# Optimization experiments

Hardware: AMD Instinct MI355X
Metric: run time of the kernel (lower is better)

## Reference

```python
import jax, jax.numpy as jnp
import numpy as np

GROUPSIZE = 128
IN_F, OUT_F = 4096, 11008
TOKENS = 512


def setup_inputs() -> dict:
    key = jax.random.key(0)
    k1, k2, k3, k4, k5 = jax.random.split(key, 5)
    x = jax.random.normal(k1, (TOKENS, IN_F), dtype=jnp.float32)
    # packed 4-bit codes: two nibbles per byte, stored as int32 in [0, 256)
    qweight = jax.random.randint(k2, (OUT_F * IN_F // 2,), 0, 256, dtype=jnp.int32)
    n_groups = OUT_F * IN_F // GROUPSIZE
    scales = jax.random.uniform(k3, (n_groups, 1), dtype=jnp.float32) * 0.02 + 1e-3
    zeros = jax.random.uniform(k4, (n_groups, 1), dtype=jnp.float32) * 15.0
    bias = jax.random.normal(k5, (OUT_F,), dtype=jnp.float32)
    return {"x": x, "qweight": qweight, "scales": scales, "zeros": zeros, "bias": bias}


def _dequant_w4(qweight, scales, zeros, dtype):
    # python_decompress: high nibble then low nibble, each in [0,16)
    hi = (qweight >> 4) % 16
    lo = qweight % 16
    codes = jnp.stack([hi, lo], axis=-1).reshape(-1, GROUPSIZE).astype(dtype)
    # group-wise dequant: (code - zero) * scale, zeros/scales are (n_groups, 1)
    w = (codes - zeros.astype(dtype)) * scales.astype(dtype)
    return w.reshape(OUT_F, IN_F)


def reference(x, qweight, scales, zeros, bias):
    w = _dequant_w4(qweight, scales, zeros, x.dtype)  # [out, in]
    return x @ w.T + bias
```

## Files before the change

kernel.cpp:

```cpp
#include <hip/hip_runtime.h>

#define GROUPSIZE 128
#define IN_F 4096
#define OUT_F 11008
#define TOKENS 512
#define N_GROUPS (OUT_F * IN_F / GROUPSIZE)

#define BM 64
#define BN 128
#define BK 64
#define NTHREADS 256
#define NT (IN_F / BK)

typedef _Float16 half8  __attribute__((ext_vector_type(8)));
typedef _Float16 half2v __attribute__((ext_vector_type(2)));
typedef float    f32x4  __attribute__((ext_vector_type(4)));
typedef int      ivec4  __attribute__((ext_vector_type(4)));

__device__ __forceinline__ int swz(int r, int k) {
    return ((r << 6) + k) ^ ((r & 7) << 3);
}

__device__ __forceinline__ void glds16(const _Float16* g, _Float16* l) {
    __builtin_amdgcn_global_load_lds(
        (const __attribute__((address_space(1))) void*)g,
        (__attribute__((address_space(3))) void*)l, 16, 0, 0);
}

__global__ __launch_bounds__(256)
void cvt_x_kernel(const float* __restrict__ x, _Float16* __restrict__ x16) {
    size_t i = ((size_t)blockIdx.x * 256 + threadIdx.x) * 8;
    f32x4 a = *(const f32x4*)(x + i);
    f32x4 b = *(const f32x4*)(x + i + 4);
    half8 h;
    h[0]=(_Float16)a[0]; h[1]=(_Float16)a[1]; h[2]=(_Float16)a[2]; h[3]=(_Float16)a[3];
    h[4]=(_Float16)b[0]; h[5]=(_Float16)b[1]; h[6]=(_Float16)b[2]; h[7]=(_Float16)b[3];
    *(half8*)(x16 + i) = h;
}

__global__ __launch_bounds__(256)
void szpack_kernel(const float* __restrict__ s, const float* __restrict__ z,
                   uint2* __restrict__ szp) {
    int g = blockIdx.x * 256 + threadIdx.x;
    if (g >= N_GROUPS) return;
    _Float16 S = (_Float16)s[g];
    _Float16 B = (_Float16)(-(64.0f + z[g]) * (float)S);
    unsigned short su = __builtin_bit_cast(unsigned short, S);
    unsigned short bu = __builtin_bit_cast(unsigned short, B);
    uint2 r;
    r.x = ((unsigned)su << 16) | su;
    r.y = ((unsigned)bu << 16) | bu;
    szp[g] = r;
}

__device__ __forceinline__ half8 dq8(ivec4 q, uint2 sz) {
    half2v S  = __builtin_bit_cast(half2v, sz.x);
    half2v Bv = __builtin_bit_cast(half2v, sz.y);
    half8 r;
#pragma unroll
    for (int e = 0; e < 4; ++e) {
        unsigned qq = (unsigned)q[e];
        unsigned u = ((qq & 0xF0u) | ((qq << 20) & 0x00F00000u)) | 0x54005400u;
        half2v h = __builtin_bit_cast(half2v, u);
        half2v w = h * S + Bv;
        r[2*e]   = w[0];
        r[2*e+1] = w[1];
    }
    return r;
}

__global__ __launch_bounds__(NTHREADS, 3)
void qlinear_main(const _Float16* __restrict__ x16,
                  const int*   __restrict__ qw,
                  const uint2* __restrict__ szp,
                  const float* __restrict__ bias,
                  float*       __restrict__ out)
{
    __shared__ __align__(16) _Float16 As[2][BM * BK];
    __shared__ __align__(16) _Float16 Bs[2][BN * BK];

    const int tid = threadIdx.x;
    const int n0 = blockIdx.x * BN;
    const int m0 = blockIdx.y * BM;
    const int wv = tid >> 6, ln = tid & 63;

    const int brow = tid & 127;
    const int bh   = tid >> 7;
    const int* qg = qw + (size_t)(n0 + brow) * (IN_F / 2) + bh * 16;
    const int szbase = (n0 + brow) * (IN_F / GROUPSIZE);

    const int ar  = wv * 16 + (ln >> 3);
    const int gsw = (ln & 7) ^ ((ln >> 3) & 7);
    const _Float16* ag = x16 + (size_t)(m0 + ar) * IN_F + gsw * 8;

    const int wr = (wv >> 1) * 32, wc = (wv & 1) * 64;
    const int lr = ln & 15, lk8 = (ln >> 4) * 8, lk4 = (ln >> 4) * 4;

    f32x4 acc[2][4];
#pragma unroll
    for (int i = 0; i < 2; ++i)
#pragma unroll
        for (int j = 0; j < 4; ++j)
            acc[i][j] = (f32x4){0.f, 0.f, 0.f, 0.f};

#define LOAD_Q(qs, szs, tt) do {                                   \
        const ivec4* qp = (const ivec4*)(qg + (tt) * 32);          \
        qs[0] = qp[0]; qs[1] = qp[1]; qs[2] = qp[2]; qs[3] = qp[3];\
        szs = szp[szbase + ((tt) >> 1)];                           \
    } while (0)

#define STAGE_A(tt, buf) do {                                      \
        const _Float16* gp = ag + (size_t)(tt) * 64;               \
        glds16(gp,             &As[buf][wv * 1024]);               \
        glds16(gp + 8 * IN_F,  &As[buf][wv * 1024 + 512]);         \
    } while (0)

#define DQ_STORE(qs, szs, buf) do {                                        \
        *(half8*)&Bs[buf][swz(brow, bh * 32 + 0)]  = dq8(qs[0], szs);      \
        *(half8*)&Bs[buf][swz(brow, bh * 32 + 8)]  = dq8(qs[1], szs);      \
        *(half8*)&Bs[buf][swz(brow, bh * 32 + 16)] = dq8(qs[2], szs);      \
        *(half8*)&Bs[buf][swz(brow, bh * 32 + 24)] = dq8(qs[3], szs);      \
    } while (0)

    auto mfma_phase = [&](int buf) {
#pragma unroll
        for (int kk = 0; kk < 2; ++kk) {
            half8 af[2], bf[4];
#pragma unroll
            for (int i = 0; i < 2; ++i)
                af[i] = *(const half8*)&As[buf][swz(wr + i * 16 + lr, kk * 32 + lk8)];
#pragma unroll
            for (int j = 0; j < 4; ++j)
                bf[j] = *(const half8*)&Bs[buf][swz(wc + j * 16 + lr, kk * 32 + lk8)];
#pragma unroll
            for (int i = 0; i < 2; ++i)
#pragma unroll
                for (int j = 0; j < 4; ++j)
                    acc[i][j] = __builtin_amdgcn_mfma_f32_16x16x32_f16(
                        af[i], bf[j], acc[i][j], 0, 0, 0);
        }
    };

    ivec4 qA[4], qB[4];
    uint2 szA, szB;
    LOAD_Q(qA, szA, 0);
    LOAD_Q(qB, szB, 1);
    STAGE_A(0, 0);
    DQ_STORE(qA, szA, 0);
    __syncthreads();

    for (int t = 0; t < NT; t += 2) {
        {
            const int tl = (t + 2 < NT) ? t + 2 : NT - 1;
            LOAD_Q(qA, szA, tl);
            STAGE_A((t + 1 < NT) ? t + 1 : NT - 1, 1);
            DQ_STORE(qB, szB, 1);
            mfma_phase(0);
            __syncthreads();
        }
        {
            const int tl = (t + 3 < NT) ? t + 3 : NT - 1;
            LOAD_Q(qB, szB, tl);
            STAGE_A((t + 2 < NT) ? t + 2 : NT - 1, 0);
            DQ_STORE(qA, szA, 0);
            mfma_phase(1);
            __syncthreads();
        }
    }

#pragma unroll
    for (int j = 0; j < 4; ++j) {
        const int col = n0 + wc + j * 16 + lr;
        const float bv = bias[col];
#pragma unroll
        for (int i = 0; i < 2; ++i) {
            const int rb = m0 + wr + i * 16 + lk4;
#pragma unroll
            for (int r = 0; r < 4; ++r)
                out[(size_t)(rb + r) * OUT_F + col] = acc[i][j][r] + bv;
        }
    }
#undef LOAD_Q
#undef STAGE_A
#undef DQ_STORE
}

extern "C" void kernel_launch(void* const* d_in, const int* in_sizes, int n_in,
                              void* d_out, int out_size, void* d_ws, size_t ws_size,
                              hipStream_t stream) {
    const float* x      = (const float*)d_in[0];
    const int*   qw     = (const int*)d_in[1];
    const float* scales = (const float*)d_in[2];
    const float* zeros  = (const float*)d_in[3];
    const float* bias   = (const float*)d_in[4];
    float*       out    = (float*)d_out;

    _Float16* x16 = (_Float16*)d_ws;
    uint2*    szp = (uint2*)((char*)d_ws + (size_t)TOKENS * IN_F * 2);

    cvt_x_kernel<<<TOKENS * IN_F / (256 * 8), 256, 0, stream>>>(x, x16);
    szpack_kernel<<<(N_GROUPS + 255) / 256, 256, 0, stream>>>(scales, zeros, szp);

    dim3 grid(OUT_F / BN, TOKENS / BM);
    qlinear_main<<<grid, NTHREADS, 0, stream>>>(x16, qw, szp, bias, out);
}
```

Baseline: 312.1 us.

## Coalesce packed weight loads and swap grid order for weight reuse

Weight loading is remapped so that 8 consecutive threads read contiguous 16-byte chunks of one row, covering 32 rows per pass with four passes, instead of each thread reading 64 contiguous bytes of its own row. Each thread now keeps four scale/zero pairs, one per row. The grid is also transposed so that the M-blocks sharing one N-tile are launched next to each other, which should improve L2 reuse of the quantized weights across token blocks. Register use goes up slightly because of the per-row scale/zero values.

Result: faster. 255.0 us (-18.3%).

```diff
diff --git a/kernel.cpp b/kernel.cpp
--- a/kernel.cpp
+++ b/kernel.cpp
@@ -80,14 +80,14 @@
     __shared__ __align__(16) _Float16 Bs[2][BN * BK];
 
     const int tid = threadIdx.x;
-    const int n0 = blockIdx.x * BN;
-    const int m0 = blockIdx.y * BM;
+    const int m0 = blockIdx.x * BM;
+    const int n0 = blockIdx.y * BN;
     const int wv = tid >> 6, ln = tid & 63;
 
-    const int brow = tid & 127;
-    const int bh   = tid >> 7;
-    const int* qg = qw + (size_t)(n0 + brow) * (IN_F / 2) + bh * 16;
-    const int szbase = (n0 + brow) * (IN_F / GROUPSIZE);
+    const int s8 = tid & 7;
+    const int r0 = tid >> 3;
+    const int* qg = qw + (size_t)(n0 + r0) * (IN_F / 2) + s8 * 4;
+    const int szb = (n0 + r0) * (IN_F / GROUPSIZE);
 
     const int ar  = wv * 16 + (ln >> 3);
     const int gsw = (ln & 7) ^ ((ln >> 3) & 7);
@@ -103,10 +103,12 @@
         for (int j = 0; j < 4; ++j)
             acc[i][j] = (f32x4){0.f, 0.f, 0.f, 0.f};
 
-#define LOAD_Q(qs, szs, tt) do {                                   \
-        const ivec4* qp = (const ivec4*)(qg + (tt) * 32);          \
-        qs[0] = qp[0]; qs[1] = qp[1]; qs[2] = qp[2]; qs[3] = qp[3];\
-        szs = szp[szbase + ((tt) >> 1)];                           \
+#define LOAD_Q(qs, szs, tt) do {                                            \
+        _Pragma("unroll")                                                   \
+        for (int j = 0; j < 4; ++j) {                                       \
+            qs[j]  = *(const ivec4*)(qg + (size_t)j * 32 * (IN_F/2) + (tt) * 32); \
+            szs[j] = szp[szb + j * 32 * (IN_F/GROUPSIZE) + ((tt) >> 1)];    \
+        }                                                                   \
     } while (0)
 
 #define STAGE_A(tt, buf) do {                                      \
@@ -116,10 +118,9 @@
     } while (0)
 
 #define DQ_STORE(qs, szs, buf) do {                                        \
-        *(half8*)&Bs[buf][swz(brow, bh * 32 + 0)]  = dq8(qs[0], szs);      \
-        *(half8*)&Bs[buf][swz(brow, bh * 32 + 8)]  = dq8(qs[1], szs);      \
-        *(half8*)&Bs[buf][swz(brow, bh * 32 + 16)] = dq8(qs[2], szs);      \
-        *(half8*)&Bs[buf][swz(brow, bh * 32 + 24)] = dq8(qs[3], szs);      \
+        _Pragma("unroll")                                                  \
+        for (int j = 0; j < 4; ++j)                                        \
+            *(half8*)&Bs[buf][swz(r0 + 32 * j, s8 * 8)] = dq8(qs[j], szs[j]); \
     } while (0)
 
     auto mfma_phase = [&](int buf) {
@@ -142,7 +143,7 @@
     };
 
     ivec4 qA[4], qB[4];
-    uint2 szA, szB;
+    uint2 szA[4], szB[4];
     LOAD_Q(qA, szA, 0);
     LOAD_Q(qB, szB, 1);
     STAGE_A(0, 0);
@@ -201,6 +202,6 @@
     cvt_x_kernel<<<TOKENS * IN_F / (256 * 8), 256, 0, stream>>>(x, x16);
     szpack_kernel<<<(N_GROUPS + 255) / 256, 256, 0, stream>>>(scales, zeros, szp);
 
-    dim3 grid(OUT_F / BN, TOKENS / BM);
+    dim3 grid(TOKENS / BM, OUT_F / BN);
     qlinear_main<<<grid, NTHREADS, 0, stream>>>(x16, qw, szp, bias, out);
 }
```
